# Performance work log

Measured on AMD Instinct MI355X. Metric: run time of the kernel, lower is better.

## Reference

```python
import jax, jax.numpy as jnp
import numpy as np

MAX_TURNS = 11      # args.max_considered_history_turns
HIDDEN = 768        # args.bert_hidden
SEQ_LEN = 512       # max_seq_length
BATCH_SIZE = 64     # args.batch_size (== len(slice_mask))
SLICE_NUM = 16      # number of real examples in the batch
ROWS = 64           # sum of real slice_mask entries = rows of the inputs


def setup_inputs() -> dict:
    key = jax.random.key(0)
    k1, k2, k3, k4 = jax.random.split(key, 4)
    # 16 real examples with 4 history turns each (sum=64=ROWS); trailing 48
    # entries of 1 consume the zero-pad rows exactly as in the torch code.
    slice_mask = jnp.array([4] * SLICE_NUM + [1] * (BATCH_SIZE - SLICE_NUM),
                           dtype=jnp.int32)
    bert_representation = jax.random.normal(k1, (ROWS, SEQ_LEN, HIDDEN), jnp.float32)
    history_attention_input = jax.random.normal(k2, (ROWS, HIDDEN), jnp.float32)
    mtl_input = jax.random.normal(k3, (ROWS, HIDDEN), jnp.float32)
    W = 0.02 * jax.random.normal(k4, (1, HIDDEN), jnp.float32)  # linear weight, init std=0.02
    b = jnp.zeros((1,), jnp.float32)                            # linear bias
    return {
        "bert_representation": bert_representation,
        "history_attention_input": history_attention_input,
        "mtl_input": mtl_input,
        "W": W,
        "b": b,
        "slice_mask": slice_mask,
        "slice_num": SLICE_NUM,
    }


def reference(bert_representation, history_attention_input, mtl_input, W, b,
              slice_mask, slice_num):
    S = int(slice_num)
    T = MAX_TURNS
    rows = history_attention_input.shape[0]

    ns = slice_mask[:S]                                  # real turn counts [S]
    offsets = jnp.concatenate([jnp.zeros((1,), ns.dtype), jnp.cumsum(ns)[:-1]])
    pad_len = T - ns                                     # left zero-padding per example
    t = jnp.arange(T, dtype=ns.dtype)
    # gather index into the flat row axis for padded tensor [S, T]
    idx = offsets[:, None] + t[None, :] - pad_len[:, None]
    valid = (t[None, :] >= pad_len[:, None])             # sequence_mask flipped
    valid_f = valid.astype(history_attention_input.dtype)
    idx_c = jnp.clip(idx, 0, rows - 1)

    # padded history input [S, T, H]; invalid slots are zeros (ZeroPad2d)
    hist_pad = history_attention_input[idx_c] * valid_f[:, :, None]
    logits = jnp.einsum('sth,oh->st', hist_pad, W) + b[0]     # [S, T]
    exp_masked = jnp.exp(logits) * valid_f
    probs = exp_masked / jnp.sum(exp_masked, axis=1, keepdims=True)  # [S, T]

    # per-row weight: each real row r belongs to example seg[r] at turn tt[r]
    r = jnp.arange(rows)
    boundaries = jnp.cumsum(ns)
    seg = jnp.searchsorted(boundaries, r, side='right')       # [rows]
    pos = r - offsets[seg]
    tt = pad_len[seg] + pos
    w = probs[seg, tt]                                        # [rows]

    new_mtl_input = jax.ops.segment_sum(mtl_input * w[:, None], seg,
                                        num_segments=S)       # [S, H]
    new_bert_representation = jax.ops.segment_sum(
        bert_representation * w[:, None, None], seg, num_segments=S)  # [S, L, H]
    return new_bert_representation, new_mtl_input, probs
```

## Files before the change

kernel.cpp:

```cpp
#include <hip/hip_runtime.h>
#include <math.h>

#define T_MAX 11

typedef float f4 __attribute__((ext_vector_type(4)));


__global__ __launch_bounds__(256) void k_probs(
    const float*  __restrict__ hist,
    const float4* __restrict__ mtl4,
    const float*  __restrict__ W,
    const float*  __restrict__ b,
    const int*    __restrict__ slice_mask,
    int S, int rows, int hidden,
    float*  __restrict__ probs_out,
    float4* __restrict__ out_mtl,
    float*  __restrict__ params)
{
    __shared__ float s_exp[64];
    __shared__ float s_wk[64];
    __shared__ int   s_off, s_n;

    const int sidx = blockIdx.x;
    const int tid  = threadIdx.x;
    const int lane = tid & 63;
    const int wave = tid >> 6;

    if (tid == 0) {
        int acc = 0, n = 0;
        for (int i = 0; i < S; ++i) {
            const int v = slice_mask[i];
            if (i < sidx) acc += v;
            if (i == sidx) n = v;
        }
        s_off = acc; s_n = n;
    }
    __syncthreads();

    const int o  = s_off;
    const int n  = s_n;
    const int h4 = hidden >> 2;
    const float4* W4 = (const float4*)W;

    for (int k = wave; k < n; k += 4) {
        const int idx = min(o + k, rows - 1);
        const float4* hrow = (const float4*)(hist + (size_t)idx * hidden);
        float acc = 0.0f;
        for (int j = lane; j < h4; j += 64) {
            const float4 hv = hrow[j];
            const float4 wv = W4[j];
            acc += hv.x*wv.x + hv.y*wv.y + hv.z*wv.z + hv.w*wv.w;
        }
        #pragma unroll
        for (int d = 32; d > 0; d >>= 1)
            acc += __shfl_down(acc, d);
        if (lane == 0) s_exp[k] = expf(acc + b[0]);
    }
    __syncthreads();

    if (tid == 0) {
        float sum = 0.0f;
        for (int k = 0; k < n; ++k) sum += s_exp[k];
        const float inv = 1.0f / sum;
        float* pp = params + sidx * 16;
        for (int k = 0; k < 12; ++k) {
            const float wk = (k < n) ? s_exp[k] * inv : 0.0f;
            s_wk[k] = wk;
            pp[k] = wk;
        }
        ((int*)pp)[12] = o;
        ((int*)pp)[13] = n;
    }
    __syncthreads();

    if (tid < T_MAX) {
        const int pad = T_MAX - n;
        probs_out[sidx * T_MAX + tid] = (tid >= pad && tid - pad < n)
                                        ? s_wk[tid - pad] : 0.0f;
    }

    for (int i = tid; i < h4; i += 256) {
        float4 acc = {0.f, 0.f, 0.f, 0.f};
        for (int k = 0; k < n; ++k) {
            const float wk = s_wk[k];
            const int r = min(o + k, rows - 1);
            const float4 v = mtl4[(size_t)r * h4 + i];
            acc.x += wk * v.x; acc.y += wk * v.y;
            acc.z += wk * v.z; acc.w += wk * v.w;
        }
        out_mtl[(size_t)sidx * h4 + i] = acc;
    }
}

__global__ __launch_bounds__(256) void k_segsum(
    const f4* __restrict__ bert,
    const float* __restrict__ params,
    int nchunks, int bert_cols4, int rows,
    f4* __restrict__ out_bert)
{
    const int sidx  = blockIdx.x / nchunks;
    const int chunk = blockIdx.x - sidx * nchunks;
    const int tid   = threadIdx.x;

    const float* pp = params + sidx * 16;
    const f4 wv = *(const f4*)pp;
    const int o = ((const int*)pp)[12];
    const int n = ((const int*)pp)[13];

    const int base = chunk * 1024 + tid;
    f4* outp = out_bert + (size_t)sidx * bert_cols4;

    if (n == 4) {
        const f4* r0 = bert + (size_t)min(o + 0, rows - 1) * bert_cols4;
        const f4* r1 = bert + (size_t)min(o + 1, rows - 1) * bert_cols4;
        const f4* r2 = bert + (size_t)min(o + 2, rows - 1) * bert_cols4;
        const f4* r3 = bert + (size_t)min(o + 3, rows - 1) * bert_cols4;

        f4 v[4][4];
        #pragma unroll
        for (int j = 0; j < 4; ++j) {
            const int i = base + j * 256;
            v[j][0] = __builtin_nontemporal_load(&r0[i]);
            v[j][1] = __builtin_nontemporal_load(&r1[i]);
            v[j][2] = __builtin_nontemporal_load(&r2[i]);
            v[j][3] = __builtin_nontemporal_load(&r3[i]);
        }
        #pragma unroll
        for (int j = 0; j < 4; ++j) {
            const int i = base + j * 256;
            f4 acc = wv.x * v[j][0] + wv.y * v[j][1]
                   + wv.z * v[j][2] + wv.w * v[j][3];
            __builtin_nontemporal_store(acc, &outp[i]);
        }
    } else if (n == 1) {
        const f4* r0 = bert + (size_t)min(o, rows - 1) * bert_cols4;
        #pragma unroll
        for (int j = 0; j < 4; ++j) {
            const int i = base + j * 256;
            const f4 acc = wv.x * __builtin_nontemporal_load(&r0[i]);
            __builtin_nontemporal_store(acc, &outp[i]);
        }
    } else {
        #pragma unroll
        for (int j = 0; j < 4; ++j) {
            const int i = base + j * 256;
            f4 acc = {0.f, 0.f, 0.f, 0.f};
            for (int k = 0; k < n; ++k) {
                const float wk = pp[min(k, 11)];
                const int r = min(o + k, rows - 1);
                acc += wk * __builtin_nontemporal_load(&bert[(size_t)r * bert_cols4 + i]);
            }
            __builtin_nontemporal_store(acc, &outp[i]);
        }
    }
}

extern "C" void kernel_launch(void* const* d_in, const int* in_sizes, int n_in,
                              void* d_out, int out_size, void* d_ws, size_t ws_size,
                              hipStream_t stream) {
    const float* bert = (const float*)d_in[0];
    const float* hist = (const float*)d_in[1];
    const float* mtl  = (const float*)d_in[2];
    const float* W    = (const float*)d_in[3];
    const float* b    = (const float*)d_in[4];
    const int* slice_mask = (const int*)d_in[5];

    const int hidden = in_sizes[3];
    const int rows   = in_sizes[1] / hidden;
    const int seq    = in_sizes[0] / (rows * hidden);
    const int S = out_size / (seq * hidden + hidden + T_MAX);

    float* out       = (float*)d_out;
    float* out_bert  = out;
    float* out_mtl   = out_bert + (size_t)S * seq * hidden;
    float* out_probs = out_mtl  + (size_t)S * hidden;

    float* params = (float*)d_ws;

    k_probs<<<S, 256, 0, stream>>>(hist, (const float4*)mtl, W, b, slice_mask,
                                   S, rows, hidden,
                                   out_probs, (float4*)out_mtl, params);

    const int bert_cols4 = seq * hidden / 4;
    const int chunk_f4   = 1024;
    const int nchunks    = (bert_cols4 + chunk_f4 - 1) / chunk_f4;
    const int grid       = S * nchunks;

    k_segsum<<<grid, 256, 0, stream>>>((const f4*)bert, params,
                                       nchunks, bert_cols4, rows,
                                       (f4*)out_bert);
}
```

Baseline: 160.7 us.

## Fuse softmax-weight kernel into segment-sum kernel, recomputing weights per block

Merges the two launches into one kernel in which every block recomputes its example's history logits, softmax weights and offsets, instead of reading them from a workspace written by a separate kernel. Only chunk 0 of each example writes probs and the mtl output. This removes one launch and the serialization between the two kernels. The cost is redundant dot products over the history rows in every block (small hist reads that mostly hit cache) and a slice_mask scan hardcoded to at most 16 entries.

```diff
diff --git a/kernel.cpp b/kernel.cpp
--- a/kernel.cpp
+++ b/kernel.cpp
@@ -5,112 +5,83 @@
 
 typedef float f4 __attribute__((ext_vector_type(4)));
 
+__global__ __launch_bounds__(256) void k_fused(
+    const f4*    __restrict__ bert,
+    const float* __restrict__ hist,
+    const f4*    __restrict__ mtl4,
+    const float* __restrict__ W,
+    const float* __restrict__ b,
+    const int*   __restrict__ slice_mask,
+    int S, int rows, int hidden,
+    int nchunks, int bert_cols4,
+    f4*    __restrict__ out_bert,
+    f4*    __restrict__ out_mtl,
+    float* __restrict__ probs_out)
+{
+    __shared__ float s_e[T_MAX + 1];
 
-__global__ __launch_bounds__(256) void k_probs(
-    const float*  __restrict__ hist,
-    const float4* __restrict__ mtl4,
-    const float*  __restrict__ W,
-    const float*  __restrict__ b,
-    const int*    __restrict__ slice_mask,
-    int S, int rows, int hidden,
-    float*  __restrict__ probs_out,
-    float4* __restrict__ out_mtl,
-    float*  __restrict__ params)
-{
-    __shared__ float s_exp[64];
-    __shared__ float s_wk[64];
-    __shared__ int   s_off, s_n;
+    const int sidx  = blockIdx.x / nchunks;
+    const int chunk = blockIdx.x - sidx * nchunks;
+    const int tid   = threadIdx.x;
+    const int lane  = tid & 63;
+    const int wave  = tid >> 6;
 
-    const int sidx = blockIdx.x;
-    const int tid  = threadIdx.x;
-    const int lane = tid & 63;
-    const int wave = tid >> 6;
+    int o = 0, n = 0;
+    #pragma unroll
+    for (int i = 0; i < 16; ++i) {
+        const int v = (i < S) ? slice_mask[i] : 0;
+        if (i < sidx)  o += v;
+        if (i == sidx) n = v;
+    }
 
-    if (tid == 0) {
-        int acc = 0, n = 0;
-        for (int i = 0; i < S; ++i) {
-            const int v = slice_mask[i];
-            if (i < sidx) acc += v;
-            if (i == sidx) n = v;
-        }
-        s_off = acc; s_n = n;
-    }
-    __syncthreads();
+    if (tid < T_MAX && tid >= n) s_e[tid] = 0.0f;
 
-    const int o  = s_off;
-    const int n  = s_n;
     const int h4 = hidden >> 2;
-    const float4* W4 = (const float4*)W;
-
+    const f4* W4 = (const f4*)W;
     for (int k = wave; k < n; k += 4) {
         const int idx = min(o + k, rows - 1);
-        const float4* hrow = (const float4*)(hist + (size_t)idx * hidden);
+        const f4* hrow = (const f4*)(hist + (size_t)idx * hidden);
         float acc = 0.0f;
         for (int j = lane; j < h4; j += 64) {
-            const float4 hv = hrow[j];
-            const float4 wv = W4[j];
-            acc += hv.x*wv.x + hv.y*wv.y + hv.z*wv.z + hv.w*wv.w;
+            const f4 hv = hrow[j];
+            const f4 wv = W4[j];
+            acc += hv.x * wv.x + hv.y * wv.y + hv.z * wv.z + hv.w * wv.w;
         }
         #pragma unroll
         for (int d = 32; d > 0; d >>= 1)
             acc += __shfl_down(acc, d);
-        if (lane == 0) s_exp[k] = expf(acc + b[0]);
+        if (lane == 0) s_e[k] = expf(acc + b[0]);
     }
     __syncthreads();
 
-    if (tid == 0) {
-        float sum = 0.0f;
-        for (int k = 0; k < n; ++k) sum += s_exp[k];
-        const float inv = 1.0f / sum;
-        float* pp = params + sidx * 16;
-        for (int k = 0; k < 12; ++k) {
-            const float wk = (k < n) ? s_exp[k] * inv : 0.0f;
-            s_wk[k] = wk;
-            pp[k] = wk;
+    float sum = 0.0f;
+    #pragma unroll
+    for (int k = 0; k < T_MAX; ++k) sum += s_e[k];
+    const float inv = 1.0f / sum;
+
+    if (chunk == 0) {
+        if (tid < T_MAX) {
+            const int pad = T_MAX - n;
+            probs_out[sidx * T_MAX + tid] =
+                (tid >= pad) ? s_e[tid - pad] * inv : 0.0f;
         }
-        ((int*)pp)[12] = o;
-        ((int*)pp)[13] = n;
+        for (int i = tid; i < h4; i += 256) {
+            f4 acc = {0.f, 0.f, 0.f, 0.f};
+            for (int k = 0; k < n; ++k) {
+                const float wk = s_e[k] * inv;
+                const int r = min(o + k, rows - 1);
+                acc += wk * mtl4[(size_t)r * h4 + i];
+            }
+            out_mtl[(size_t)sidx * h4 + i] = acc;
+        }
     }
-    __syncthreads();
-
-    if (tid < T_MAX) {
-        const int pad = T_MAX - n;
-        probs_out[sidx * T_MAX + tid] = (tid >= pad && tid - pad < n)
-                                        ? s_wk[tid - pad] : 0.0f;
-    }
-
-    for (int i = tid; i < h4; i += 256) {
-        float4 acc = {0.f, 0.f, 0.f, 0.f};
-        for (int k = 0; k < n; ++k) {
-            const float wk = s_wk[k];
-            const int r = min(o + k, rows - 1);
-            const float4 v = mtl4[(size_t)r * h4 + i];
-            acc.x += wk * v.x; acc.y += wk * v.y;
-            acc.z += wk * v.z; acc.w += wk * v.w;
-        }
-        out_mtl[(size_t)sidx * h4 + i] = acc;
-    }
-}
-
-__global__ __launch_bounds__(256) void k_segsum(
-    const f4* __restrict__ bert,
-    const float* __restrict__ params,
-    int nchunks, int bert_cols4, int rows,
-    f4* __restrict__ out_bert)
-{
-    const int sidx  = blockIdx.x / nchunks;
-    const int chunk = blockIdx.x - sidx * nchunks;
-    const int tid   = threadIdx.x;
-
-    const float* pp = params + sidx * 16;
-    const f4 wv = *(const f4*)pp;
-    const int o = ((const int*)pp)[12];
-    const int n = ((const int*)pp)[13];
 
     const int base = chunk * 1024 + tid;
     f4* outp = out_bert + (size_t)sidx * bert_cols4;
 
     if (n == 4) {
+        const float w0 = s_e[0] * inv, w1 = s_e[1] * inv;
+        const float w2 = s_e[2] * inv, w3 = s_e[3] * inv;
         const f4* r0 = bert + (size_t)min(o + 0, rows - 1) * bert_cols4;
         const f4* r1 = bert + (size_t)min(o + 1, rows - 1) * bert_cols4;
         const f4* r2 = bert + (size_t)min(o + 2, rows - 1) * bert_cols4;
@@ -128,16 +99,16 @@
         #pragma unroll
         for (int j = 0; j < 4; ++j) {
             const int i = base + j * 256;
-            f4 acc = wv.x * v[j][0] + wv.y * v[j][1]
-                   + wv.z * v[j][2] + wv.w * v[j][3];
+            f4 acc = w0 * v[j][0] + w1 * v[j][1] + w2 * v[j][2] + w3 * v[j][3];
             __builtin_nontemporal_store(acc, &outp[i]);
         }
     } else if (n == 1) {
+        const float w0 = s_e[0] * inv;
         const f4* r0 = bert + (size_t)min(o, rows - 1) * bert_cols4;
         #pragma unroll
         for (int j = 0; j < 4; ++j) {
             const int i = base + j * 256;
-            const f4 acc = wv.x * __builtin_nontemporal_load(&r0[i]);
+            const f4 acc = w0 * __builtin_nontemporal_load(&r0[i]);
             __builtin_nontemporal_store(acc, &outp[i]);
         }
     } else {
@@ -146,7 +117,7 @@
             const int i = base + j * 256;
             f4 acc = {0.f, 0.f, 0.f, 0.f};
             for (int k = 0; k < n; ++k) {
-                const float wk = pp[min(k, 11)];
+                const float wk = s_e[min(k, T_MAX - 1)] * inv;
                 const int r = min(o + k, rows - 1);
                 acc += wk * __builtin_nontemporal_load(&bert[(size_t)r * bert_cols4 + i]);
             }
@@ -175,18 +146,14 @@
     float* out_mtl   = out_bert + (size_t)S * seq * hidden;
     float* out_probs = out_mtl  + (size_t)S * hidden;
 
-    float* params = (float*)d_ws;
-
-    k_probs<<<S, 256, 0, stream>>>(hist, (const float4*)mtl, W, b, slice_mask,
-                                   S, rows, hidden,
-                                   out_probs, (float4*)out_mtl, params);
-
     const int bert_cols4 = seq * hidden / 4;
     const int chunk_f4   = 1024;
     const int nchunks    = (bert_cols4 + chunk_f4 - 1) / chunk_f4;
     const int grid       = S * nchunks;
 
-    k_segsum<<<grid, 256, 0, stream>>>((const f4*)bert, params,
-                                       nchunks, bert_cols4, rows,
-                                       (f4*)out_bert);
+    k_fused<<<grid, 256, 0, stream>>>((const f4*)bert, hist, (const f4*)mtl,
+                                      W, b, slice_mask,
+                                      S, rows, hidden,
+                                      nchunks, bert_cols4,
+                                      (f4*)out_bert, (f4*)out_mtl, out_probs);
 }
```

Result: faster. 156.6 us (-2.6%).
